# Kernel optimization log

Hardware: AMD Instinct MI355X
Metric: run time of the kernel (lower is better)

The kernel has to match this reference:

```python
import jax, jax.numpy as jnp
import numpy as np

DIM_IN, DIM_K, DIM_V = 1024, 1024, 1024

def setup_inputs() -> dict:
    key = jax.random.key(0)
    k1, k2, k3, k4 = jax.random.split(key, 4)
    x = jax.random.normal(k1, (4, 2048, DIM_IN), dtype=jnp.float32)
    # Linear(dim_in, dim_k, bias=False): store as [in, out] for x @ W
    Wq = jax.random.normal(k2, (DIM_IN, DIM_K), dtype=jnp.float32) * (1.0 / np.sqrt(DIM_IN))
    Wk = jax.random.normal(k3, (DIM_IN, DIM_K), dtype=jnp.float32) * (1.0 / np.sqrt(DIM_IN))
    Wv = jax.random.normal(k4, (DIM_IN, DIM_V), dtype=jnp.float32) * (1.0 / np.sqrt(DIM_IN))
    return {"x": x, "Wq": Wq, "Wk": Wk, "Wv": Wv, "causal_mask": 1}

def reference(x, Wq, Wk, Wv, causal_mask):
    # x: [b, n, dim_in]
    b, n, _ = x.shape
    q = jnp.einsum('bnd,dk->bnk', x, Wq)
    k = jnp.einsum('bnd,dk->bnk', x, Wk)
    v = jnp.einsum('bnd,dv->bnv', x, Wv)
    scale = 1.0 / np.sqrt(Wq.shape[1])
    dist = jnp.einsum('bik,bjk->bij', q, k) * scale  # [b, n, n]
    if causal_mask:
        mask = jnp.tril(jnp.ones((n, n), dtype=bool))
        dist = jnp.where(mask, dist, -jnp.inf)
    attn = jax.nn.softmax(dist, axis=-1)
    return jnp.einsum('bij,bjv->biv', attn, v)  # [b, n, dim_v]
```

## Files before the change

### kernel.cpp

```cpp
#include <hip/hip_runtime.h>
#include <hip/hip_bf16.h>
#include <stdint.h>

#define BM 128
#define BN 128
#define BK 64

typedef __attribute__((ext_vector_type(8))) short bf16x8;
typedef __attribute__((ext_vector_type(4))) float floatx4;


__device__ __forceinline__ unsigned short f2bf(float f) {
    unsigned int x;
    __builtin_memcpy(&x, &f, 4);
    unsigned int r = (x + 0x7fffu + ((x >> 16) & 1u)) >> 16;
    return (unsigned short)r;
}

__device__ __forceinline__ float bf2f_hi(unsigned int u_hi_masked) {
    float f;
    __builtin_memcpy(&f, &u_hi_masked, 4);
    return f;
}

__device__ __forceinline__ void async_copy16(const void* g, void* l) {
    __builtin_amdgcn_global_load_lds(
        (const __attribute__((address_space(1))) void*)(uintptr_t)g,
        (__attribute__((address_space(3))) void*)(uint32_t)(uintptr_t)l,
        16, 0, 0);
}


__global__ __launch_bounds__(256) void prep(const float* __restrict__ x,
                                            const float* __restrict__ Wq,
                                            const float* __restrict__ Wk,
                                            const float* __restrict__ Wv,
                                            unsigned short* __restrict__ xb,
                                            unsigned short* __restrict__ wT) {
    __shared__ float tile[32][33];
    int bid = blockIdx.x;
    int tid = threadIdx.x;
    if (bid < 8192) {
        int i = bid * 256 + tid;
        float4 v = ((const float4*)x)[i];
        ushort4 o;
        o.x = f2bf(v.x);
        o.y = f2bf(v.y);
        o.z = f2bf(v.z);
        o.w = f2bf(v.w);
        ((ushort4*)xb)[i] = o;
    } else {
        int w = bid - 8192;
        int z = w >> 10;
        int r = w & 1023;
        int bx = (r & 31) * 32;
        int by = (r >> 5) * 32;
        const float* W = z == 0 ? Wq : (z == 1 ? Wk : Wv);
        int tx = tid & 31, ty = tid >> 5;
        for (int rr = 0; rr < 32; rr += 8)
            tile[ty + rr][tx] = W[(size_t)(by + ty + rr) * 1024 + bx + tx];
        __syncthreads();
        unsigned short* o = wT + (size_t)z * 1024 * 1024;
        for (int rr = 0; rr < 32; rr += 8)
            o[(size_t)(bx + ty + rr) * 1024 + by + tx] = f2bf(tile[tx][ty + rr]);
    }
}


#define SEG_STRIDE 544
#define BUF_SH (16 * SEG_STRIDE)


__device__ __forceinline__ void gemm_core(const unsigned short* __restrict__ A,
                                          int lda,
                                          const unsigned short* __restrict__ B,
                                          int ldb, void* __restrict__ C,
                                          int ldc, bool out_bf16, int kend,
                                          float scale, int m0, int n0) {
    __shared__ __align__(16) unsigned short As[BUF_SH];
    __shared__ __align__(16) unsigned short Bs[BUF_SH];

    int tid = threadIdx.x;
    int lane = tid & 63;
    int wave = tid >> 6;
    int wm = (wave >> 1) * 64;
    int wn = (wave & 1) * 64;
    int fr = lane & 15;
    int kq = lane >> 4;

    floatx4 acc[4][4] = {};

    for (int k0 = 0; k0 < kend; k0 += BK) {
#pragma unroll
        for (int q = 0; q < 4; q++) {
            int s = 4 * q + wave;
            int r = s * 8 + (lane >> 3);
            int ko = (lane & 7) * 8;
            int dst = s * SEG_STRIDE + lane * 8;
            async_copy16(A + (size_t)(m0 + r) * lda + k0 + ko, &As[dst]);
            async_copy16(B + (size_t)(n0 + r) * ldb + k0 + ko, &Bs[dst]);
        }
        __syncthreads();

#pragma unroll
        for (int kh = 0; kh < 2; kh++) {
            int kc = kh * 4 + kq;
            bf16x8 af[4], bfg[4];
#pragma unroll
            for (int mi = 0; mi < 4; mi++) {
                int row = wm + mi * 16 + fr;
                af[mi] = *(const bf16x8*)&As[(row >> 3) * SEG_STRIDE +
                                             (row & 7) * 64 + kc * 8];
            }
#pragma unroll
            for (int ni = 0; ni < 4; ni++) {
                int row = wn + ni * 16 + fr;
                bfg[ni] = *(const bf16x8*)&Bs[(row >> 3) * SEG_STRIDE +
                                              (row & 7) * 64 + kc * 8];
            }
#pragma unroll
            for (int mi = 0; mi < 4; mi++)
#pragma unroll
                for (int ni = 0; ni < 4; ni++)
                    acc[mi][ni] = __builtin_amdgcn_mfma_f32_16x16x32_bf16(
                        af[mi], bfg[ni], acc[mi][ni], 0, 0, 0);
        }
        __syncthreads();
    }

    int col0 = n0 + wn + fr;
    int rbase = m0 + wm + kq * 4;
    if (out_bf16) {
        unsigned short* Cb = (unsigned short*)C;
#pragma unroll
        for (int mi = 0; mi < 4; mi++)
#pragma unroll
            for (int ni = 0; ni < 4; ni++)
#pragma unroll
                for (int r = 0; r < 4; r++)
                    Cb[(size_t)(rbase + mi * 16 + r) * ldc + col0 + ni * 16] =
                        f2bf(acc[mi][ni][r] * scale);
    } else {
        float* Cb = (float*)C;
#pragma unroll
        for (int mi = 0; mi < 4; mi++)
#pragma unroll
            for (int ni = 0; ni < 4; ni++)
#pragma unroll
                for (int r = 0; r < 4; r++)
                    Cb[(size_t)(rbase + mi * 16 + r) * ldc + col0 + ni * 16] =
                        acc[mi][ni][r] * scale;
    }
}


__device__ __forceinline__ void gemm_core_db(
    const unsigned short* __restrict__ A, int lda,
    const unsigned short* __restrict__ B, int ldb, void* __restrict__ C,
    int ldc, bool out_bf16, int kend, float scale, int m0, int n0) {
    __shared__ __align__(16) unsigned short As[2 * BUF_SH];
    __shared__ __align__(16) unsigned short Bs[2 * BUF_SH];

    int tid = threadIdx.x;
    int lane = tid & 63;
    int wave = tid >> 6;
    int wm = (wave >> 1) * 64;
    int wn = (wave & 1) * 64;
    int fr = lane & 15;
    int kq = lane >> 4;

    floatx4 acc[4][4] = {};

    auto stage = [&](int buf, int k0) {
#pragma unroll
        for (int q = 0; q < 4; q++) {
            int s = 4 * q + wave;
            int r = s * 8 + (lane >> 3);
            int ko = (lane & 7) * 8;
            int dst = buf * BUF_SH + s * SEG_STRIDE + lane * 8;
            async_copy16(A + (size_t)(m0 + r) * lda + k0 + ko, &As[dst]);
            async_copy16(B + (size_t)(n0 + r) * ldb + k0 + ko, &Bs[dst]);
        }
    };

    auto compute = [&](int buf) {
        const unsigned short* as = &As[buf * BUF_SH];
        const unsigned short* bs = &Bs[buf * BUF_SH];
#pragma unroll
        for (int kh = 0; kh < 2; kh++) {
            int kc = kh * 4 + kq;
            bf16x8 af[4], bfg[4];
#pragma unroll
            for (int mi = 0; mi < 4; mi++) {
                int row = wm + mi * 16 + fr;
                af[mi] = *(const bf16x8*)&as[(row >> 3) * SEG_STRIDE +
                                             (row & 7) * 64 + kc * 8];
            }
#pragma unroll
            for (int ni = 0; ni < 4; ni++) {
                int row = wn + ni * 16 + fr;
                bfg[ni] = *(const bf16x8*)&bs[(row >> 3) * SEG_STRIDE +
                                              (row & 7) * 64 + kc * 8];
            }
#pragma unroll
            for (int mi = 0; mi < 4; mi++)
#pragma unroll
                for (int ni = 0; ni < 4; ni++)
                    acc[mi][ni] = __builtin_amdgcn_mfma_f32_16x16x32_bf16(
                        af[mi], bfg[ni], acc[mi][ni], 0, 0, 0);
        }
    };

    stage(0, 0);
    __syncthreads();
    int nt = kend / BK;
    int cur = 0;
    for (int t = 0; t < nt; t++) {
        if (t + 1 < nt) stage(cur ^ 1, (t + 1) * BK);
        compute(cur);
        __syncthreads();
        cur ^= 1;
    }

    int col0 = n0 + wn + fr;
    int rbase = m0 + wm + kq * 4;
    if (out_bf16) {
        unsigned short* Cb = (unsigned short*)C;
#pragma unroll
        for (int mi = 0; mi < 4; mi++)
#pragma unroll
            for (int ni = 0; ni < 4; ni++)
#pragma unroll
                for (int r = 0; r < 4; r++)
                    Cb[(size_t)(rbase + mi * 16 + r) * ldc + col0 + ni * 16] =
                        f2bf(acc[mi][ni][r] * scale);
    } else {
        float* Cb = (float*)C;
#pragma unroll
        for (int mi = 0; mi < 4; mi++)
#pragma unroll
            for (int ni = 0; ni < 4; ni++)
#pragma unroll
                for (int r = 0; r < 4; r++)
                    Cb[(size_t)(rbase + mi * 16 + r) * ldc + col0 + ni * 16] =
                        acc[mi][ni][r] * scale;
    }
}


__global__ __launch_bounds__(512, 2) void gemm_qk8(
    const unsigned short* __restrict__ A, const unsigned short* __restrict__ B,
    unsigned short* __restrict__ C) {
    __shared__ __align__(16) unsigned short lds[4][16384];

    const int tid = threadIdx.x;
    const int lane = tid & 63;
    const int wave = tid >> 6;
    const int wr = wave >> 2;
    const int wc = wave & 3;
    const int fr = lane & 15;
    const int kq = lane >> 4;
    const int m0 = blockIdx.y * 256;
    const int n0 = blockIdx.x * 256;

    const unsigned short* aS0 =
        A + (size_t)(m0 + wave * 32 + (lane >> 2)) * 1024 + (lane & 3) * 8;
    const unsigned short* aS1 = aS0 + 16 * 1024;
    const unsigned short* bS0 =
        B + (size_t)(n0 + wave * 32 + (lane >> 2)) * 1024 + (lane & 3) * 8;
    const unsigned short* bS1 = bS0 + 16 * 1024;
    const int dA0 = wave * 1024 + lane * 8;
    const int dA1 = dA0 + 512;
    const int dB0 = 8192 + dA0;
    const int dB1 = 8192 + dA1;

    floatx4 acc[8][4] = {};

    auto stageA = [&](int j) {
        unsigned short* d = &lds[j & 3][0];
        int kk = j * 32;
        async_copy16(aS0 + kk, d + dA0);
        async_copy16(aS1 + kk, d + dA1);
    };
    auto stageB = [&](int j) {
        unsigned short* d = &lds[j & 3][0];
        int kk = j * 32;
        async_copy16(bS0 + kk, d + dB0);
        async_copy16(bS1 + kk, d + dB1);
    };

    stageA(0); stageB(0);
    stageA(1); stageB(1);
    stageA(2); stageB(2);

    for (int j = 0; j < 32; ++j) {
        if (j < 30) {
            asm volatile("s_waitcnt vmcnt(8)" ::: "memory");
        } else if (j == 30) {
            asm volatile("s_waitcnt vmcnt(4)" ::: "memory");
        } else {
            asm volatile("s_waitcnt vmcnt(0)" ::: "memory");
        }
        asm volatile("s_barrier" ::: "memory");

        const unsigned short* as = &lds[j & 3][0];
        const unsigned short* bs = as + 8192;
        bf16x8 af[4], bfr[4];

#pragma unroll
        for (int mi = 0; mi < 4; mi++)
            af[mi] = *(const bf16x8*)&as[(wr * 128 + mi * 16 + fr) * 32 + kq * 8];
#pragma unroll
        for (int ni = 0; ni < 4; ni++)
            bfr[ni] = *(const bf16x8*)&bs[(wc * 64 + ni * 16 + fr) * 32 + kq * 8];
        if (j + 3 < 32) stageA(j + 3);
        __builtin_amdgcn_s_setprio(1);
#pragma unroll
        for (int mi = 0; mi < 4; mi++)
#pragma unroll
            for (int ni = 0; ni < 4; ni++)
                acc[mi][ni] = __builtin_amdgcn_mfma_f32_16x16x32_bf16(
                    af[mi], bfr[ni], acc[mi][ni], 0, 0, 0);
        __builtin_amdgcn_s_setprio(0);

#pragma unroll
        for (int mi = 0; mi < 4; mi++)
            af[mi] = *(const bf16x8*)&as[(wr * 128 + 64 + mi * 16 + fr) * 32 +
                                         kq * 8];
#pragma unroll
        for (int ni = 0; ni < 4; ni++)
            bfr[ni] = *(const bf16x8*)&bs[(wc * 64 + ni * 16 + fr) * 32 + kq * 8];
        if (j + 3 < 32) stageB(j + 3);
        __builtin_amdgcn_s_setprio(1);
#pragma unroll
        for (int mi = 0; mi < 4; mi++)
#pragma unroll
            for (int ni = 0; ni < 4; ni++)
                acc[4 + mi][ni] = __builtin_amdgcn_mfma_f32_16x16x32_bf16(
                    af[mi], bfr[ni], acc[4 + mi][ni], 0, 0, 0);
        __builtin_amdgcn_s_setprio(0);
    }

    const int col0 = n0 + wc * 64 + fr;
    const int rbase = m0 + wr * 128 + kq * 4;
#pragma unroll
    for (int a = 0; a < 8; a++)
#pragma unroll
        for (int ni = 0; ni < 4; ni++)
#pragma unroll
            for (int r = 0; r < 4; r++)
                C[(size_t)(rbase + a * 16 + r) * 2048 + col0 + ni * 16] =
                    f2bf(acc[a][ni][r]);
}


__device__ __forceinline__ void tri_decode(int r2, int& mb, int& nb) {
    mb = (int)((sqrtf(8.0f * r2 + 1.0f) - 1.0f) * 0.5f);
    while ((mb + 1) * (mb + 2) / 2 <= r2) mb++;
    while (mb * (mb + 1) / 2 > r2) mb--;
    nb = r2 - mb * (mb + 1) / 2;
}


__global__ __launch_bounds__(256, 4) void s_vt(
    const unsigned short* __restrict__ qk, unsigned short* __restrict__ S,
    const unsigned short* __restrict__ wTv,
    const unsigned short* __restrict__ xb, unsigned short* __restrict__ vt) {
    int bid = blockIdx.x;
    int job = (bid & 7) * 132 + (bid >> 3);
    const unsigned short *A, *B;
    void* C;
    int lda, ldb, ldc, m0, n0;
    float scale;
    if (job < 544) {
        int bz = job / 136;
        int mb, nb;
        tri_decode(job - bz * 136, mb, nb);
        const unsigned short* Q = qk + (size_t)bz * 2048 * 2048;
        A = Q;
        lda = 2048;
        B = Q + 1024;
        ldb = 2048;
        C = S + (size_t)bz * 2048 * 2048;
        ldc = 2048;
        scale = 0.03125f;
        m0 = mb * BM;
        n0 = nb * BN;
    } else {
        int v = job - 544;
        A = wTv;
        lda = 1024;
        B = xb;
        ldb = 1024;
        C = vt;
        ldc = 8192;
        scale = 1.0f;
        m0 = (v >> 6) * BM;
        n0 = (v & 63) * BN;
    }
    gemm_core(A, lda, B, ldb, C, ldc, true, 1024, scale, m0, n0);
}


__global__ __launch_bounds__(256) void sm(unsigned short* __restrict__ S) {
    int lane = threadIdx.x & 63;
    int row = blockIdx.x * 4 + (threadIdx.x >> 6);
    int i = row & 2047;
    int nc = i >> 9;
    unsigned short* s = S + (size_t)row * 2048;

    uint4 raw[4];
#pragma unroll
    for (int c = 0; c < 4; c++) {
        raw[c] = make_uint4(0u, 0u, 0u, 0u);
        if (c <= nc) raw[c] = ((const uint4*)s)[lane + c * 64];
    }

    const float NEG = -1.0e30f;
    float p[32];
    float m = NEG;
#pragma unroll
    for (int c = 0; c < 4; c++) {
        const unsigned int* u = (const unsigned int*)&raw[c];
#pragma unroll
        for (int w = 0; w < 4; w++) {
            int j = c * 512 + lane * 8 + w * 2;
            float f0 = bf2f_hi(u[w] << 16);
            float f1 = bf2f_hi(u[w] & 0xffff0000u);
            f0 = (j <= i) ? f0 : NEG;
            f1 = (j + 1 <= i) ? f1 : NEG;
            p[c * 8 + w * 2] = f0;
            p[c * 8 + w * 2 + 1] = f1;
            m = fmaxf(m, fmaxf(f0, f1));
        }
    }
#pragma unroll
    for (int o = 32; o > 0; o >>= 1) m = fmaxf(m, __shfl_xor(m, o));

    float sum = 0.f;
#pragma unroll
    for (int t = 0; t < 32; t++) {
        p[t] = __expf(p[t] - m);
        sum += p[t];
    }
#pragma unroll
    for (int o = 32; o > 0; o >>= 1) sum += __shfl_xor(sum, o);
    float inv = 1.0f / sum;

#pragma unroll
    for (int c = 0; c < 4; c++) {
        if (c > nc) continue;
        uint4 out;
        unsigned int* u = (unsigned int*)&out;
#pragma unroll
        for (int w = 0; w < 4; w++) {
            unsigned int lo = f2bf(p[c * 8 + w * 2] * inv);
            unsigned int hi = f2bf(p[c * 8 + w * 2 + 1] * inv);
            u[w] = lo | (hi << 16);
        }
        ((uint4*)s)[lane + c * 64] = out;
    }
}


__global__ __launch_bounds__(256, 4) void gemm_pv(
    const unsigned short* __restrict__ S, const unsigned short* __restrict__ vt,
    float* __restrict__ out) {
    int b = blockIdx.x;
    int c = b & 255;
    int nb = c >> 5;
    int s = c & 31;
    int bz = s & 3;
    int mbase = s >> 2;
    int mb = (b < 256) ? mbase : 15 - mbase;
    int kend = (mb + 1) * 128;
    gemm_core_db(S + (size_t)bz * 2048 * 2048, 2048, vt + (size_t)bz * 2048,
                 8192, out + (size_t)bz * 2048 * 1024, 1024, false, kend, 1.0f,
                 mb * BM, nb * BN);
}


extern "C" void kernel_launch(void* const* d_in, const int* in_sizes, int n_in,
                              void* d_out, int out_size, void* d_ws,
                              size_t ws_size, hipStream_t stream) {
    const float* x = (const float*)d_in[0];
    const float* Wq = (const float*)d_in[1];
    const float* Wk = (const float*)d_in[2];
    const float* Wv = (const float*)d_in[3];

    char* ws = (char*)d_ws;
    unsigned short* qk = (unsigned short*)(ws);
    unsigned short* S = (unsigned short*)(ws + 33554432);
    unsigned short* vt = (unsigned short*)(ws + 67108864);
    unsigned short* xb = (unsigned short*)(ws + 83886080);
    unsigned short* wT = (unsigned short*)(ws + 100663296);

    prep<<<11264, 256, 0, stream>>>(x, Wq, Wk, Wv, xb, wT);
    gemm_qk8<<<dim3(8, 32), 512, 0, stream>>>(xb, wT, qk);
    s_vt<<<1056, 256, 0, stream>>>(qk, S, wT + 2 * 1024 * 1024, xb, vt);
    sm<<<2048, 256, 0, stream>>>(S);
    gemm_pv<<<512, 256, 0, stream>>>(S, vt, (float*)d_out);
}
```

Measured before the change: 221.7 us.

## Double-buffer GEMM shared-memory tiles with 32-wide K steps

Replaces the single-buffered BK=64 GEMM core with a two-buffer pipeline over K=32 slices. The next slice is copied asynchronously while MFMAs run on the current one, so there is one barrier per step instead of two. The padded segment layout is replaced by a plain 128x32 layout, which may bring LDS bank conflicts. It also doubles the number of loop iterations and halves the compute available per barrier to hide latency.

```diff
diff --git a/kernel.cpp b/kernel.cpp
--- a/kernel.cpp
+++ b/kernel.cpp
@@ -71,14 +71,12 @@
 #define BUF_SH (16 * SEG_STRIDE)
 
 
-__device__ __forceinline__ void gemm_core(const unsigned short* __restrict__ A,
-                                          int lda,
-                                          const unsigned short* __restrict__ B,
-                                          int ldb, void* __restrict__ C,
-                                          int ldc, bool out_bf16, int kend,
-                                          float scale, int m0, int n0) {
-    __shared__ __align__(16) unsigned short As[BUF_SH];
-    __shared__ __align__(16) unsigned short Bs[BUF_SH];
+__device__ __forceinline__ void gemm_core_db32(
+    const unsigned short* __restrict__ A, int lda,
+    const unsigned short* __restrict__ B, int ldb, void* __restrict__ C,
+    int ldc, bool out_bf16, int kend, float scale, int m0, int n0) {
+    __shared__ __align__(16) unsigned short As[2][128 * 32];
+    __shared__ __align__(16) unsigned short Bs[2][128 * 32];
 
     int tid = threadIdx.x;
     int lane = tid & 63;
@@ -90,42 +88,42 @@
 
     floatx4 acc[4][4] = {};
 
-    for (int k0 = 0; k0 < kend; k0 += BK) {
-#pragma unroll
-        for (int q = 0; q < 4; q++) {
-            int s = 4 * q + wave;
-            int r = s * 8 + (lane >> 3);
-            int ko = (lane & 7) * 8;
-            int dst = s * SEG_STRIDE + lane * 8;
-            async_copy16(A + (size_t)(m0 + r) * lda + k0 + ko, &As[dst]);
-            async_copy16(B + (size_t)(n0 + r) * ldb + k0 + ko, &Bs[dst]);
+    auto stage = [&](int buf, int k0) {
+#pragma unroll
+        for (int p = 0; p < 2; p++) {
+            int idx = tid + p * 256;
+            int r = idx >> 2;
+            int co = (idx & 3) * 8;
+            async_copy16(A + (size_t)(m0 + r) * lda + k0 + co, &As[buf][idx * 8]);
+            async_copy16(B + (size_t)(n0 + r) * ldb + k0 + co, &Bs[buf][idx * 8]);
         }
+    };
+
+    auto compute = [&](int buf) {
+        bf16x8 af[4], bfg[4];
+#pragma unroll
+        for (int mi = 0; mi < 4; mi++)
+            af[mi] = *(const bf16x8*)&As[buf][(wm + mi * 16 + fr) * 32 + kq * 8];
+#pragma unroll
+        for (int ni = 0; ni < 4; ni++)
+            bfg[ni] = *(const bf16x8*)&Bs[buf][(wn + ni * 16 + fr) * 32 + kq * 8];
+#pragma unroll
+        for (int mi = 0; mi < 4; mi++)
+#pragma unroll
+            for (int ni = 0; ni < 4; ni++)
+                acc[mi][ni] = __builtin_amdgcn_mfma_f32_16x16x32_bf16(
+                    af[mi], bfg[ni], acc[mi][ni], 0, 0, 0);
+    };
+
+    stage(0, 0);
+    __syncthreads();
+    int nt = kend / 32;
+    int cur = 0;
+    for (int t = 0; t < nt; t++) {
+        if (t + 1 < nt) stage(cur ^ 1, (t + 1) * 32);
+        compute(cur);
         __syncthreads();
-
-#pragma unroll
-        for (int kh = 0; kh < 2; kh++) {
-            int kc = kh * 4 + kq;
-            bf16x8 af[4], bfg[4];
-#pragma unroll
-            for (int mi = 0; mi < 4; mi++) {
-                int row = wm + mi * 16 + fr;
-                af[mi] = *(const bf16x8*)&As[(row >> 3) * SEG_STRIDE +
-                                             (row & 7) * 64 + kc * 8];
-            }
-#pragma unroll
-            for (int ni = 0; ni < 4; ni++) {
-                int row = wn + ni * 16 + fr;
-                bfg[ni] = *(const bf16x8*)&Bs[(row >> 3) * SEG_STRIDE +
-                                              (row & 7) * 64 + kc * 8];
-            }
-#pragma unroll
-            for (int mi = 0; mi < 4; mi++)
-#pragma unroll
-                for (int ni = 0; ni < 4; ni++)
-                    acc[mi][ni] = __builtin_amdgcn_mfma_f32_16x16x32_bf16(
-                        af[mi], bfg[ni], acc[mi][ni], 0, 0, 0);
-        }
-        __syncthreads();
+        cur ^= 1;
     }
 
     int col0 = n0 + wn + fr;
@@ -398,7 +396,7 @@
         m0 = (v >> 6) * BM;
         n0 = (v & 63) * BN;
     }
-    gemm_core(A, lda, B, ldb, C, ldc, true, 1024, scale, m0, n0);
+    gemm_core_db32(A, lda, B, ldb, C, ldc, true, 1024, scale, m0, n0);
 }
 
 
```

Measured after the change: 229.4 us. 1.03x slower.
